# Kernel optimization log

Hardware: AMD Instinct MI355X
Metric: run time of the kernel (lower is better)

The kernel has to match this reference:

```python
import jax, jax.numpy as jnp
import numpy as np

N_NODES = 50000
N_EDGES = 800000
HIDDEN = 128


def setup_inputs() -> dict:
    key = jax.random.key(0)
    k_h, k_src, k_dst, k_w1, k_w2 = jax.random.split(key, 5)
    h = jax.random.normal(k_h, (N_NODES, HIDDEN), dtype=jnp.float32)
    src = jax.random.randint(k_src, (N_EDGES,), 0, N_NODES, dtype=jnp.int32)
    dst = jax.random.randint(k_dst, (N_EDGES,), 0, N_NODES, dtype=jnp.int32)
    edge_index = jnp.stack([src, dst], axis=0)
    # MLP params (torch Linear: y = x @ W.T + b); store as [in, out] for einsum
    s1 = 1.0 / np.sqrt(2 * HIDDEN)
    s2 = 1.0 / np.sqrt(HIDDEN)
    W1 = jax.random.uniform(k_w1, (2 * HIDDEN, HIDDEN), jnp.float32, -s1, s1)
    b1 = jnp.zeros((HIDDEN,), jnp.float32)
    W2 = jax.random.uniform(k_w2, (HIDDEN, HIDDEN), jnp.float32, -s2, s2)
    b2 = jnp.zeros((HIDDEN,), jnp.float32)
    return {"h": h, "edge_index": edge_index, "W1": W1, "b1": b1, "W2": W2, "b2": b2}


def reference(h, edge_index, W1, b1, W2, b2):
    src, dst = edge_index[0], edge_index[1]
    n = h.shape[0]
    # scatter-add of gathered source features -> agg [N, H]
    agg = jax.ops.segment_sum(h[src], dst, num_segments=n)
    # degree normalization (clamp_min 1)
    deg = jax.ops.segment_sum(jnp.ones_like(dst, dtype=h.dtype), dst, num_segments=n)
    deg = jnp.maximum(deg, 1.0)[:, None]
    agg = agg / deg
    x = jnp.concatenate([h, agg], axis=1)  # [N, 2H]
    x = jax.nn.relu(x @ W1 + b1)
    x = jax.nn.relu(x @ W2 + b2)
    return x
```

## Files before the change

### kernel.cpp

```cpp
#include <hip/hip_runtime.h>

typedef unsigned short u16;
typedef unsigned int u32;
typedef __attribute__((ext_vector_type(8))) short short8;
typedef __attribute__((ext_vector_type(4))) float f32x4;
typedef __attribute__((ext_vector_type(4))) u32 u32x4;

#define BKT_SHIFT 6
#define BKT_NODES 64
#define CAP 1536
#define EPB 4096
#define NBH 1024

__device__ inline u16 f2bf(float f){ u32 u=__float_as_uint(f); u32 r=((u>>16)&1u)+0x7fffu; return (u16)((u+r)>>16); }

__global__ __launch_bounds__(256) void k_castbin(
    const int* __restrict__ src, const int* __restrict__ dst,
    int* __restrict__ gcnt, u32* __restrict__ recs_g, int nE, int gB,
    const float* __restrict__ h, u16* __restrict__ hbf, int nh8,
    const float* __restrict__ w1, const float* __restrict__ w2,
    u16* __restrict__ w1t, u16* __restrict__ w2t){
  __shared__ u32 rl[EPB];
  __shared__ int hist[NBH];
  __shared__ int curs[NBH];
  int t = threadIdx.x;
  if ((int)blockIdx.x < gB){
    int e0 = blockIdx.x*EPB;
    for (int i=t;i<NBH;i+=256) hist[i]=0;
    __syncthreads();
    #pragma unroll
    for (int i=0;i<EPB/256;i++){
      int e = e0 + i*256 + t;
      u32 rec = 0xffffffffu;
      if (e < nE){
        u32 d = (u32)dst[e];
        u32 s = (u32)src[e];
        u32 bb = d >> BKT_SHIFT;
        rec = (bb<<22) | ((d & (u32)(BKT_NODES-1))<<16) | s;
        atomicAdd(&hist[bb & (NBH-1)], 1);
      }
      rl[i*256+t] = rec;
    }
    __syncthreads();
    for (int i=t;i<NBH;i+=256){
      int c = hist[i];
      curs[i] = c ? atomicAdd(&gcnt[i], c) : 0;
    }
    __syncthreads();
    #pragma unroll
    for (int i=0;i<EPB/256;i++){
      u32 rec = rl[i*256+t];
      if (rec != 0xffffffffu){
        u32 bb = rec>>22;
        int slot = atomicAdd(&curs[bb], 1);
        if (slot < CAP) recs_g[(size_t)bb*CAP + slot] = rec & 0x3fffffu;
      }
    }
  } else {
    int e = ((int)blockIdx.x - gB)*256 + t;
    if (e < nh8){
      float4 a = *(const float4*)(h + (size_t)e*8);
      float4 b = *(const float4*)(h + (size_t)e*8 + 4);
      u32x4 p;
      p.x = (u32)f2bf(a.x) | ((u32)f2bf(a.y)<<16);
      p.y = (u32)f2bf(a.z) | ((u32)f2bf(a.w)<<16);
      p.z = (u32)f2bf(b.x) | ((u32)f2bf(b.y)<<16);
      p.w = (u32)f2bf(b.z) | ((u32)f2bf(b.w)<<16);
      *(u32x4*)(hbf + (size_t)e*8) = p;
    }
    if (e < 256*128){ int k=e>>7, nn=e&127; w1t[nn*256+k]=f2bf(w1[e]); }
    else { int j=e-256*128; if (j<128*128){ int k=j>>7, nn=j&127; w2t[nn*128+k]=f2bf(w2[j]); } }
  }
}

__global__ __launch_bounds__(512, 6) void k_aggmlp(
    const u16* __restrict__ hbf, const u32* __restrict__ recs_g,
    const int* __restrict__ gcnt,
    const u16* __restrict__ w1t, const u16* __restrict__ w2t,
    const float* __restrict__ b1, const float* __restrict__ b2,
    float* __restrict__ out, int n){
  __shared__ __align__(16) u16 xs[64*264];
  __shared__ u16 srt[CAP];
  __shared__ int hist[BKT_NODES];
  __shared__ int scn[BKT_NODES];
  __shared__ int cur[BKT_NODES];
  int b = blockIdx.x, t = threadIdx.x;
  int node0 = b*BKT_NODES;
  int cnt = gcnt[b]; if (cnt > CAP) cnt = CAP;
  const u32* rp = recs_g + (size_t)b*CAP;

  if (t < BKT_NODES) hist[t] = 0;
  #pragma unroll
  for (int i=0;i<4;i++){
    int idx = i*512 + t;
    int row = idx>>5, c8 = idx&31;
    int node = node0 + row;
    u32x4 v = {0,0,0,0};
    if (node < n && c8 < 16) v = *(const u32x4*)(hbf + (size_t)node*128 + c8*8);
    *(u32x4*)(&xs[row*264 + c8*8]) = v;
  }
  __syncthreads();
  for (int i=t; i<cnt; i+=512) atomicAdd(&hist[(rp[i]>>16)&(BKT_NODES-1)], 1);
  __syncthreads();
  if (t < BKT_NODES){
    int v = hist[t];
    int s = v;
    #pragma unroll
    for (int d=1; d<64; d<<=1){
      int o = __shfl_up(s, d, 64);
      if (t >= d) s += o;
    }
    scn[t] = s;
    cur[t] = s - v;
  }
  __syncthreads();
  for (int i=t; i<cnt; i+=512){
    u32 r = rp[i];
    int slot = atomicAdd(&cur[(r>>16)&(BKT_NODES-1)], 1);
    srt[slot] = (u16)(r & 0xffffu);
  }
  __syncthreads();

  int grp = t>>4, l16g = t&15;
  #pragma unroll
  for (int i=0;i<2;i++){
    int nl = i*32 + grp;
    int deg = hist[nl];
    int st  = scn[nl] - deg;
    float a[8] = {0.f,0.f,0.f,0.f,0.f,0.f,0.f,0.f};
    for (int base=0; base<deg; base+=8){
      int sidx[8];
      #pragma unroll
      for (int j=0;j<8;j++){
        int jj = base + j; if (jj > deg-1) jj = deg-1;
        sidx[j] = srt[st + jj];
      }
      u32x4 vv[8];
      #pragma unroll
      for (int j=0;j<8;j++)
        vv[j] = *(const u32x4*)(hbf + (size_t)sidx[j]*128 + l16g*8);
      #pragma unroll
      for (int j=0;j<8;j++){
        float m = (base+j < deg) ? 1.f : 0.f;
        #pragma unroll
        for (int q=0;q<4;q++){
          u32 u = vv[j][q];
          union{u32 v; float f;} lo,hi; lo.v=u<<16; hi.v=u&0xffff0000u;
          a[q*2]   += m*lo.f;
          a[q*2+1] += m*hi.f;
        }
      }
    }
    float inv = 1.f/(float)(deg>0?deg:1);
    u32x4 o;
    o.x = (u32)f2bf(a[0]*inv) | ((u32)f2bf(a[1]*inv)<<16);
    o.y = (u32)f2bf(a[2]*inv) | ((u32)f2bf(a[3]*inv)<<16);
    o.z = (u32)f2bf(a[4]*inv) | ((u32)f2bf(a[5]*inv)<<16);
    o.w = (u32)f2bf(a[6]*inv) | ((u32)f2bf(a[7]*inv)<<16);
    *(u32x4*)(&xs[nl*264 + 128 + l16g*8]) = o;
  }

  int wave=t>>6, lane=t&63, quad=lane>>4, l16=lane&15;
  const u16* w1p = w1t + (size_t)(wave*16 + l16)*256 + quad*8;
  short8 wb1[8];
  #pragma unroll
  for (int ks=0;ks<8;ks++) wb1[ks] = *(const short8*)(w1p + ks*32);
  __syncthreads();

  f32x4 acc[4];
  #pragma unroll
  for (int m=0;m<4;m++) acc[m]=(f32x4){0,0,0,0};
  #pragma unroll
  for (int ks=0;ks<8;ks++){
    #pragma unroll
    for (int m=0;m<4;m++){
      short8 av = *(const short8*)(&xs[(m*16+l16)*264 + ks*32 + quad*8]);
      acc[m] = __builtin_amdgcn_mfma_f32_16x16x32_bf16(av, wb1[ks], acc[m],0,0,0);
    }
  }

  const u16* w2p = w2t + (size_t)(wave*16 + l16)*128 + quad*8;
  short8 wb2[4];
  #pragma unroll
  for (int ks=0;ks<4;ks++) wb2[ks] = *(const short8*)(w2p + ks*32);
  __syncthreads();

  float bias = b1[wave*16 + l16];
  #pragma unroll
  for (int m=0;m<4;m++){
    #pragma unroll
    for (int r=0;r<4;r++){
      int row = m*16 + quad*4 + r;
      float v0 = acc[m][r] + bias; v0 = v0>0.f ? v0 : 0.f;
      xs[row*264 + wave*16 + l16] = f2bf(v0);
    }
  }
  __syncthreads();

  f32x4 acc2[4];
  #pragma unroll
  for (int m=0;m<4;m++) acc2[m]=(f32x4){0,0,0,0};
  #pragma unroll
  for (int ks=0;ks<4;ks++){
    #pragma unroll
    for (int m=0;m<4;m++){
      short8 av = *(const short8*)(&xs[(m*16+l16)*264 + ks*32 + quad*8]);
      acc2[m] = __builtin_amdgcn_mfma_f32_16x16x32_bf16(av, wb2[ks], acc2[m],0,0,0);
    }
  }
  float c0 = b2[wave*16 + l16];
  #pragma unroll
  for (int m=0;m<4;m++){
    #pragma unroll
    for (int r=0;r<4;r++){
      int node = node0 + m*16 + quad*4 + r;
      if (node<n){
        float v0 = acc2[m][r]+c0; v0 = v0>0.f?v0:0.f;
        out[(size_t)node*128 + wave*16 + l16] = v0;
      }
    }
  }
}

extern "C" void kernel_launch(void* const* d_in, const int* in_sizes, int n_in,
                              void* d_out, int out_size, void* d_ws, size_t ws_size,
                              hipStream_t stream){
  const float* h  = (const float*)d_in[0];
  const int*   ei = (const int*)d_in[1];
  const float* W1 = (const float*)d_in[2];
  const float* b1 = (const float*)d_in[3];
  const float* W2 = (const float*)d_in[4];
  const float* b2 = (const float*)d_in[5];
  float* out = (float*)d_out;
  int n  = in_sizes[0] / 128;
  int nE = in_sizes[1] / 2;
  const int* srcI = ei;
  const int* dstI = ei + nE;
  int nbuck = (n + BKT_NODES - 1) >> BKT_SHIFT;

  char* ws = (char*)d_ws;
  u32* recs = (u32*)ws;
  size_t off = (size_t)nbuck*CAP*4;
  int* gcnt = (int*)(ws + off); off += 4096;
  u16* hbf  = (u16*)(ws + off); off += (size_t)n*256;
  off = (off + 15) & ~(size_t)15;
  u16* w1t  = (u16*)(ws + off);
  u16* w2t  = (u16*)(ws + off + 65536);

  hipMemsetAsync(gcnt, 0, NBH*sizeof(int), stream);
  int gB = (nE + EPB - 1)/EPB;
  int nh8 = n*16;
  int castN = nh8 > 49152 ? nh8 : 49152;
  int gC = (castN + 255)/256;
  k_castbin<<<gB+gC, 256, 0, stream>>>(srcI, dstI, gcnt, recs, nE, gB,
                                       h, hbf, nh8, W1, W2, w1t, w2t);
  k_aggmlp<<<nbuck, 512, 0, stream>>>(hbf, recs, gcnt, w1t, w2t, b1, b2, out, n);
}
```

Measured before the change: 148.5 us.

## Double-buffer neighbor gathers and stage bucket records in LDS

The neighbor aggregation loop now keeps two register buffers of eight gathered rows, so the loads for the next group are issued while the current group is being accumulated. Edge records are read from global memory once into a shared staging array and reused by the counting-sort scatter pass, instead of being loaded twice. The launch-bounds occupancy hint drops from 6 to 4 to leave room for the extra registers, and the extra 6 KB of shared memory may also reduce the number of resident blocks.

```diff
diff --git a/kernel.cpp b/kernel.cpp
--- a/kernel.cpp
+++ b/kernel.cpp
@@ -73,13 +73,23 @@
   }
 }
 
-__global__ __launch_bounds__(512, 6) void k_aggmlp(
+#define G_ISSUE(buf, g) { int base_=(g)*8; \
+  _Pragma("unroll") for (int j=0;j<8;j++){ int jj_=base_+j; if (jj_>deg-1) jj_=deg-1; \
+    buf[j] = *(const u32x4*)(hbf + (size_t)srt[st+jj_]*128 + l16g*8); } }
+#define G_ACC(buf, g) { int base_=(g)*8; \
+  _Pragma("unroll") for (int j=0;j<8;j++){ float m_=(base_+j<deg)?1.f:0.f; \
+    _Pragma("unroll") for (int q=0;q<4;q++){ u32 u_=buf[j][q]; \
+      union{u32 v; float f;} lo_,hi_; lo_.v=u_<<16; hi_.v=u_&0xffff0000u; \
+      a[q*2]+=m_*lo_.f; a[q*2+1]+=m_*hi_.f; } } }
+
+__global__ __launch_bounds__(512, 4) void k_aggmlp(
     const u16* __restrict__ hbf, const u32* __restrict__ recs_g,
     const int* __restrict__ gcnt,
     const u16* __restrict__ w1t, const u16* __restrict__ w2t,
     const float* __restrict__ b1, const float* __restrict__ b2,
     float* __restrict__ out, int n){
   __shared__ __align__(16) u16 xs[64*264];
+  __shared__ u32 stage[CAP];
   __shared__ u16 srt[CAP];
   __shared__ int hist[BKT_NODES];
   __shared__ int scn[BKT_NODES];
@@ -100,7 +110,11 @@
     *(u32x4*)(&xs[row*264 + c8*8]) = v;
   }
   __syncthreads();
-  for (int i=t; i<cnt; i+=512) atomicAdd(&hist[(rp[i]>>16)&(BKT_NODES-1)], 1);
+  for (int i=t; i<cnt; i+=512){
+    u32 r = rp[i];
+    stage[i] = r;
+    atomicAdd(&hist[(r>>16)&(BKT_NODES-1)], 1);
+  }
   __syncthreads();
   if (t < BKT_NODES){
     int v = hist[t];
@@ -115,7 +129,7 @@
   }
   __syncthreads();
   for (int i=t; i<cnt; i+=512){
-    u32 r = rp[i];
+    u32 r = stage[i];
     int slot = atomicAdd(&cur[(r>>16)&(BKT_NODES-1)], 1);
     srt[slot] = (u16)(r & 0xffffu);
   }
@@ -128,27 +142,20 @@
     int deg = hist[nl];
     int st  = scn[nl] - deg;
     float a[8] = {0.f,0.f,0.f,0.f,0.f,0.f,0.f,0.f};
-    for (int base=0; base<deg; base+=8){
-      int sidx[8];
-      #pragma unroll
-      for (int j=0;j<8;j++){
-        int jj = base + j; if (jj > deg-1) jj = deg-1;
-        sidx[j] = srt[st + jj];
-      }
-      u32x4 vv[8];
-      #pragma unroll
-      for (int j=0;j<8;j++)
-        vv[j] = *(const u32x4*)(hbf + (size_t)sidx[j]*128 + l16g*8);
-      #pragma unroll
-      for (int j=0;j<8;j++){
-        float m = (base+j < deg) ? 1.f : 0.f;
-        #pragma unroll
-        for (int q=0;q<4;q++){
-          u32 u = vv[j][q];
-          union{u32 v; float f;} lo,hi; lo.v=u<<16; hi.v=u&0xffff0000u;
-          a[q*2]   += m*lo.f;
-          a[q*2+1] += m*hi.f;
-        }
+    int nb = (deg+7)>>3;
+    if (nb){
+      u32x4 A[8], B[8];
+      G_ISSUE(A, 0);
+      int g = 0;
+      while (true){
+        if (g+1 < nb) G_ISSUE(B, g+1);
+        G_ACC(A, g);
+        g++;
+        if (g >= nb) break;
+        if (g+1 < nb) G_ISSUE(A, g+1);
+        G_ACC(B, g);
+        g++;
+        if (g >= nb) break;
       }
     }
     float inv = 1.f/(float)(deg>0?deg:1);
```

After: 150.9 us. No clear change (+1.6%).

## Split fused aggregate-MLP kernel into sort, wave-per-node gather, and MLP kernels

Applied to the files above, without the earlier changes.

Breaks the single fused bucket kernel into three launches. The first sorts each bucket's edge records by destination and writes a per-node (start, degree) table. The second uses one full wave per node for the neighbour gather, staging the bf16 mean in the unused upper half of the output buffer. The third runs the two MFMA layers reading h and that staged aggregate, which aims to give the latency-bound gather more parallelism and occupancy than the register-heavy fused kernel allowed. In exchange it adds two launches and an extra global round trip for the sorted indices and the aggregate.

```diff
diff --git a/kernel.cpp b/kernel.cpp
--- a/kernel.cpp
+++ b/kernel.cpp
@@ -73,98 +73,111 @@
   }
 }
 
-__global__ __launch_bounds__(512, 6) void k_aggmlp(
-    const u16* __restrict__ hbf, const u32* __restrict__ recs_g,
-    const int* __restrict__ gcnt,
+__global__ __launch_bounds__(256) void k_sortscat(
+    const u32* __restrict__ recs_g, const int* __restrict__ gcnt,
+    u16* __restrict__ srt_g, u32* __restrict__ nd_g, int n){
+  __shared__ u32 stage[CAP];
+  __shared__ __align__(4) u16 srt[CAP];
+  __shared__ int hist[BKT_NODES];
+  __shared__ int scn[BKT_NODES];
+  __shared__ int cur[BKT_NODES];
+  int b = blockIdx.x, t = threadIdx.x;
+  int cnt = gcnt[b]; if (cnt > CAP) cnt = CAP;
+  const u32* rp = recs_g + (size_t)b*CAP;
+  if (t < BKT_NODES) hist[t] = 0;
+  __syncthreads();
+  for (int i=t; i<cnt; i+=256){
+    u32 r = rp[i];
+    stage[i] = r;
+    atomicAdd(&hist[(r>>16)&(BKT_NODES-1)], 1);
+  }
+  __syncthreads();
+  if (t < BKT_NODES){
+    int v = hist[t];
+    int s = v;
+    #pragma unroll
+    for (int d=1; d<64; d<<=1){
+      int o = __shfl_up(s, d, 64);
+      if (t >= d) s += o;
+    }
+    scn[t] = s;
+    cur[t] = s - v;
+  }
+  __syncthreads();
+  for (int i=t; i<cnt; i+=256){
+    u32 r = stage[i];
+    int slot = atomicAdd(&cur[(r>>16)&(BKT_NODES-1)], 1);
+    srt[slot] = (u16)(r & 0xffffu);
+  }
+  __syncthreads();
+  const u32* sw = (const u32*)srt;
+  u32* gw = (u32*)(srt_g + (size_t)b*CAP);
+  for (int i=t; i<CAP/2; i+=256) gw[i] = sw[i];
+  if (t < BKT_NODES){
+    int node = b*BKT_NODES + t;
+    if (node < n) nd_g[node] = (u32)(scn[t]-hist[t]) | ((u32)hist[t]<<16);
+  }
+}
+
+__global__ __launch_bounds__(256) void k_agg(
+    const u32* __restrict__ hbfw, const u16* __restrict__ srt_g,
+    const u32* __restrict__ nd_g, u32* __restrict__ outw, int n){
+  int node = (int)((blockIdx.x*256 + threadIdx.x) >> 6);
+  int lane = threadIdx.x & 63;
+  if (node >= n) return;
+  u32 nd = nd_g[node];
+  int st  = (int)(nd & 0xffffu);
+  int deg = (int)(nd >> 16);
+  const u16* sp = srt_g + (size_t)(node>>6)*CAP + st;
+  float a0=0.f, a1=0.f;
+  for (int base=0; base<deg; base+=16){
+    int sidx[16];
+    #pragma unroll
+    for (int j=0;j<16;j++){
+      int jj = base + j; if (jj > deg-1) jj = deg-1;
+      sidx[j] = sp[jj];
+    }
+    u32 vv[16];
+    #pragma unroll
+    for (int j=0;j<16;j++) vv[j] = hbfw[(size_t)sidx[j]*64 + lane];
+    #pragma unroll
+    for (int j=0;j<16;j++){
+      float m = (base+j < deg) ? 1.f : 0.f;
+      union{u32 u; float f;} lo,hi; lo.u=vv[j]<<16; hi.u=vv[j]&0xffff0000u;
+      a0 += m*lo.f; a1 += m*hi.f;
+    }
+  }
+  float inv = 1.f/(float)(deg>0?deg:1);
+  outw[(size_t)node*128 + 64 + lane] = (u32)f2bf(a0*inv) | ((u32)f2bf(a1*inv)<<16);
+}
+
+__global__ __launch_bounds__(512) void k_mlp(
+    const u16* __restrict__ hbf, const u32* __restrict__ outw_in,
     const u16* __restrict__ w1t, const u16* __restrict__ w2t,
     const float* __restrict__ b1, const float* __restrict__ b2,
     float* __restrict__ out, int n){
   __shared__ __align__(16) u16 xs[64*264];
-  __shared__ u16 srt[CAP];
-  __shared__ int hist[BKT_NODES];
-  __shared__ int scn[BKT_NODES];
-  __shared__ int cur[BKT_NODES];
-  int b = blockIdx.x, t = threadIdx.x;
-  int node0 = b*BKT_NODES;
-  int cnt = gcnt[b]; if (cnt > CAP) cnt = CAP;
-  const u32* rp = recs_g + (size_t)b*CAP;
-
-  if (t < BKT_NODES) hist[t] = 0;
+  int t = threadIdx.x;
+  int node0 = blockIdx.x*64;
+  int wave=t>>6, lane=t&63, quad=lane>>4, l16=lane&15;
+
+  const u16* w1p = w1t + (size_t)(wave*16 + l16)*256 + quad*8;
+  short8 wb1[8];
+  #pragma unroll
+  for (int ks=0;ks<8;ks++) wb1[ks] = *(const short8*)(w1p + ks*32);
+
   #pragma unroll
   for (int i=0;i<4;i++){
     int idx = i*512 + t;
     int row = idx>>5, c8 = idx&31;
     int node = node0 + row;
     u32x4 v = {0,0,0,0};
-    if (node < n && c8 < 16) v = *(const u32x4*)(hbf + (size_t)node*128 + c8*8);
+    if (node < n){
+      if (c8 < 16) v = *(const u32x4*)(hbf + (size_t)node*128 + c8*8);
+      else         v = *(const u32x4*)(outw_in + (size_t)node*128 + 64 + (c8-16)*4);
+    }
     *(u32x4*)(&xs[row*264 + c8*8]) = v;
   }
-  __syncthreads();
-  for (int i=t; i<cnt; i+=512) atomicAdd(&hist[(rp[i]>>16)&(BKT_NODES-1)], 1);
-  __syncthreads();
-  if (t < BKT_NODES){
-    int v = hist[t];
-    int s = v;
-    #pragma unroll
-    for (int d=1; d<64; d<<=1){
-      int o = __shfl_up(s, d, 64);
-      if (t >= d) s += o;
-    }
-    scn[t] = s;
-    cur[t] = s - v;
-  }
-  __syncthreads();
-  for (int i=t; i<cnt; i+=512){
-    u32 r = rp[i];
-    int slot = atomicAdd(&cur[(r>>16)&(BKT_NODES-1)], 1);
-    srt[slot] = (u16)(r & 0xffffu);
-  }
-  __syncthreads();
-
-  int grp = t>>4, l16g = t&15;
-  #pragma unroll
-  for (int i=0;i<2;i++){
-    int nl = i*32 + grp;
-    int deg = hist[nl];
-    int st  = scn[nl] - deg;
-    float a[8] = {0.f,0.f,0.f,0.f,0.f,0.f,0.f,0.f};
-    for (int base=0; base<deg; base+=8){
-      int sidx[8];
-      #pragma unroll
-      for (int j=0;j<8;j++){
-        int jj = base + j; if (jj > deg-1) jj = deg-1;
-        sidx[j] = srt[st + jj];
-      }
-      u32x4 vv[8];
-      #pragma unroll
-      for (int j=0;j<8;j++)
-        vv[j] = *(const u32x4*)(hbf + (size_t)sidx[j]*128 + l16g*8);
-      #pragma unroll
-      for (int j=0;j<8;j++){
-        float m = (base+j < deg) ? 1.f : 0.f;
-        #pragma unroll
-        for (int q=0;q<4;q++){
-          u32 u = vv[j][q];
-          union{u32 v; float f;} lo,hi; lo.v=u<<16; hi.v=u&0xffff0000u;
-          a[q*2]   += m*lo.f;
-          a[q*2+1] += m*hi.f;
-        }
-      }
-    }
-    float inv = 1.f/(float)(deg>0?deg:1);
-    u32x4 o;
-    o.x = (u32)f2bf(a[0]*inv) | ((u32)f2bf(a[1]*inv)<<16);
-    o.y = (u32)f2bf(a[2]*inv) | ((u32)f2bf(a[3]*inv)<<16);
-    o.z = (u32)f2bf(a[4]*inv) | ((u32)f2bf(a[5]*inv)<<16);
-    o.w = (u32)f2bf(a[6]*inv) | ((u32)f2bf(a[7]*inv)<<16);
-    *(u32x4*)(&xs[nl*264 + 128 + l16g*8]) = o;
-  }
-
-  int wave=t>>6, lane=t&63, quad=lane>>4, l16=lane&15;
-  const u16* w1p = w1t + (size_t)(wave*16 + l16)*256 + quad*8;
-  short8 wb1[8];
-  #pragma unroll
-  for (int ks=0;ks<8;ks++) wb1[ks] = *(const short8*)(w1p + ks*32);
   __syncthreads();
 
   f32x4 acc[4];
@@ -232,6 +245,7 @@
   const float* W2 = (const float*)d_in[4];
   const float* b2 = (const float*)d_in[5];
   float* out = (float*)d_out;
+  u32* outw  = (u32*)d_out;
   int n  = in_sizes[0] / 128;
   int nE = in_sizes[1] / 2;
   const int* srcI = ei;
@@ -243,6 +257,10 @@
   size_t off = (size_t)nbuck*CAP*4;
   int* gcnt = (int*)(ws + off); off += 4096;
   u16* hbf  = (u16*)(ws + off); off += (size_t)n*256;
+  off = (off + 15) & ~(size_t)15;
+  u16* srt_g = (u16*)(ws + off); off += (size_t)nbuck*CAP*2;
+  off = (off + 15) & ~(size_t)15;
+  u32* nd_g = (u32*)(ws + off); off += (size_t)((n+63)&~63)*4;
   off = (off + 15) & ~(size_t)15;
   u16* w1t  = (u16*)(ws + off);
   u16* w2t  = (u16*)(ws + off + 65536);
@@ -254,5 +272,7 @@
   int gC = (castN + 255)/256;
   k_castbin<<<gB+gC, 256, 0, stream>>>(srcI, dstI, gcnt, recs, nE, gB,
                                        h, hbf, nh8, W1, W2, w1t, w2t);
-  k_aggmlp<<<nbuck, 512, 0, stream>>>(hbf, recs, gcnt, w1t, w2t, b1, b2, out, n);
-}
+  k_sortscat<<<nbuck, 256, 0, stream>>>(recs, gcnt, srt_g, nd_g, n);
+  k_agg<<<(n+3)/4, 256, 0, stream>>>((const u32*)hbf, srt_g, nd_g, outw, n);
+  k_mlp<<<nbuck, 512, 0, stream>>>(hbf, outw, w1t, w2t, b1, b2, out, n);
+}
```

Result: slower. 154.1 us (+3.8%).
